# Kernel optimization log

Hardware: AMD Instinct MI355X
Metric: run time of the kernel (lower is better)

## Reference

```python
import jax, jax.numpy as jnp
import numpy as np

IMG_H, IMG_W = 512.0, 512.0
PRE_NMS = 2000   # training-mode pre_nms_top_n
POST_NMS = 2000  # training-mode post_nms_top_n
NMS_THRESH = 0.7
SCORE_THRESH = 0.0
MIN_SIZE = 0.001


def setup_inputs() -> dict:
    key = jax.random.key(0)
    k1, k2, k3 = jax.random.split(key, 3)
    N = 8
    num_anchors_per_level = (49152, 12288, 3072, 768, 192)  # strides 4..64, 3 anchors/loc on 512^2
    A = sum(num_anchors_per_level)
    cxy = jax.random.uniform(k1, (N, A, 2), minval=0.0, maxval=512.0)
    wh = jax.random.uniform(k2, (N, A, 2), minval=2.0, maxval=120.0)
    proposals = jnp.concatenate([cxy - wh / 2, cxy + wh / 2], axis=-1)  # xyxy
    objectness = jax.random.normal(k3, (N, A), dtype=jnp.float32)
    return {"proposals": proposals, "objectness": objectness,
            "num_anchors_per_level": num_anchors_per_level}


def _box_iou(a, b):
    # a: [K,4], b: [K,4] -> [K,K] pairwise IoU (torchvision box_iou semantics)
    area_a = (a[:, 2] - a[:, 0]) * (a[:, 3] - a[:, 1])
    area_b = (b[:, 2] - b[:, 0]) * (b[:, 3] - b[:, 1])
    lt = jnp.maximum(a[:, None, :2], b[None, :, :2])
    rb = jnp.minimum(a[:, None, 2:], b[None, :, 2:])
    wh = jnp.clip(rb - lt, 0.0)
    inter = wh[..., 0] * wh[..., 1]
    return inter / (area_a[:, None] + area_b[None, :] - inter)


def _per_image(boxes, scores, lvl):
    # boxes [K,4] xyxy, scores [K] (sigmoid probs), lvl [K] int32 level ids
    # 1) clip to image
    x = jnp.clip(boxes[:, 0::2], 0.0, IMG_W)
    y = jnp.clip(boxes[:, 1::2], 0.0, IMG_H)
    boxes = jnp.stack([x[:, 0], y[:, 0], x[:, 1], y[:, 1]], axis=-1)
    # 2) small-box + 3) score-threshold masks (masking instead of boolean indexing)
    ws = boxes[:, 2] - boxes[:, 0]
    hs = boxes[:, 3] - boxes[:, 1]
    valid = (ws >= MIN_SIZE) & (hs >= MIN_SIZE) & (scores >= SCORE_THRESH)
    # 4) batched NMS: offset boxes per level so levels never overlap
    off = lvl.astype(boxes.dtype) * (jnp.max(boxes) + 1.0)
    off_boxes = boxes + off[:, None]
    sm = jnp.where(valid, scores, -jnp.inf)
    order = jnp.argsort(-sm)                 # descending score, invalid last
    boxes_s = boxes[order]
    scores_s = scores[order]
    valid_s = valid[order]
    ob_s = jax.lax.stop_gradient(off_boxes[order])
    K = ob_s.shape[0]
    iou = _box_iou(ob_s, ob_s)               # [K,K], keep decision is non-differentiable
    j = jnp.arange(K)
    def body(i, keep):
        suppress = keep[i] & (iou[i] > NMS_THRESH) & (j > i)
        return keep & ~suppress
    keep = jax.lax.fori_loop(0, K, body, valid_s)
    # 5) top post_nms kept boxes, padded to fixed size with zeros
    rank = jnp.cumsum(keep.astype(jnp.int32)) - 1
    sel_key = jnp.where(keep & (rank < POST_NMS), rank, K)
    idx = jnp.argsort(sel_key)[:POST_NMS]
    out_valid = sel_key[idx] < K
    out_boxes = jnp.where(out_valid[:, None], boxes_s[idx], 0.0)
    out_scores = jnp.where(out_valid, scores_s[idx], 0.0)
    return out_boxes, out_scores


def _forward(proposals, objectness, num_anchors_per_level):
    N = proposals.shape[0]
    napl = [int(n) for n in num_anchors_per_level]
    # per-level, per-image top-k on objectness (get_top_n_idx)
    idx_list, lv_list, off = [], [], 0
    for i, n in enumerate(napl):
        k = min(PRE_NMS, n)
        _, ti = jax.lax.top_k(objectness[:, off:off + n], k)
        idx_list.append(ti + off)
        lv_list.append(jnp.full((k,), i, dtype=jnp.int32))
        off += n
    top_idx = jnp.concatenate(idx_list, axis=1)   # [N, K_total]
    lvls = jnp.concatenate(lv_list)               # [K_total], same for every image
    bidx = jnp.arange(N)[:, None]
    obj = objectness[bidx, top_idx]
    props = proposals[bidx, top_idx]
    scores = jax.nn.sigmoid(obj)
    return jax.vmap(lambda b, s: _per_image(b, s, lvls))(props, scores)


def reference(proposals, objectness, num_anchors_per_level):
    # returns (boxes [N, POST_NMS, 4], scores [N, POST_NMS]); invalid slots zero-padded
    return _forward(proposals, objectness, num_anchors_per_level)
```

## Files before the change

### kernel.cpp

```cpp
#include <hip/hip_runtime.h>
#include <math.h>

#define NIMG 8
#define ATOT 65472
#define KTOT 6960
#define POST 2000
#define TILES_PER_IMG 1668
#define NTILES (NIMG*TILES_PER_IMG)
#define ESEG 1024
#define M_TIE 0.7000000178813934326171875
#define PAD(i) ((i) + ((i) >> 5))
#define WAVE_SYNC() asm volatile("s_waitcnt lgkmcnt(0)" ::: "memory")

__constant__ int c_NAPL[5]  = {49152,12288,3072,768,192};
__constant__ int c_LOFF[5]  = {0,49152,61440,64512,65280};
__constant__ int c_KSEL[5]  = {2000,2000,2000,768,192};
__constant__ int c_CBASE[5] = {0,2000,4000,6000,6768};
__constant__ int c_GLVL[5]  = {32,32,32,12,3};
__constant__ int c_TILEPFX[6] = {0,528,1056,1584,1662,1668};

typedef float v2f __attribute__((ext_vector_type(2)));

__device__ __forceinline__ v2f vmin2(v2f a, v2f b){
#if __has_builtin(__builtin_elementwise_min)
  return __builtin_elementwise_min(a, b);
#else
  v2f r; r.x = fminf(a.x, b.x); r.y = fminf(a.y, b.y); return r;
#endif
}
__device__ __forceinline__ v2f vmax2(v2f a, v2f b){
#if __has_builtin(__builtin_elementwise_max)
  return __builtin_elementwise_max(a, b);
#else
  v2f r; r.x = fmaxf(a.x, b.x); r.y = fmaxf(a.y, b.y); return r;
#endif
}

__device__ __forceinline__ unsigned f2u(float f){
  unsigned b = __float_as_uint(f);
  return (b & 0x80000000u) ? ~b : (b | 0x80000000u);
}
__device__ __forceinline__ unsigned long long mkkey(unsigned u, unsigned gidx){
  return ((unsigned long long)u << 32) | (unsigned long long)(0xFFFFFFFFu - gidx);
}
__device__ __forceinline__ unsigned long long shflx64(unsigned long long v, int m){
  int lo = __shfl_xor((int)(unsigned)v, m);
  int hi = __shfl_xor((int)(unsigned)(v >> 32), m);
  return ((unsigned long long)(unsigned)hi << 32) | (unsigned)lo;
}
__device__ __forceinline__ unsigned long long bstep(unsigned long long v, int elem,
                                                    int size, int st){
  unsigned long long p = shflx64(v, st);
  bool lower = (elem & st) == 0;
  bool desc  = (elem & size) == 0;
  bool takeMax = (lower == desc);
  bool gt = v > p;
  return (takeMax == gt) ? v : p;
}
__device__ __forceinline__ unsigned wsuffix(unsigned v, int lane){
  #pragma unroll
  for (int off = 1; off < 64; off <<= 1){
    unsigned p = __shfl_down(v, off);
    if (lane + off < 64) v += p;
  }
  return v;
}

extern "C" __global__ void __launch_bounds__(1024)
k_select(const float* __restrict__ prop, const float* __restrict__ obj,
         unsigned long long* __restrict__ cand, float4* __restrict__ cbox,
         unsigned* __restrict__ zzone, float4* __restrict__ out4, int out_n4){
  __shared__ unsigned long long sb[2112];
  __shared__ unsigned hist[4096];
  __shared__ unsigned h8[256];
  __shared__ unsigned wsum[16];
  __shared__ unsigned s_b12, s_cumAbove, s_t20, s_cnt;
  int task = blockIdx.x, img = task/5, lvl = task%5;
  int n = c_NAPL[lvl], k = c_KSEL[lvl], tid = threadIdx.x;
  int lane = tid & 63, wv = tid >> 6;
  if (task == 0)
    for (int i = tid; i < 1280; i += 1024) zzone[i] = 0u;
  {
    int z = task*1024 + tid;
    if (z < out_n4) out4[z] = make_float4(0.f,0.f,0.f,0.f);
  }

  const float4* o4 = (const float4*)(obj + (size_t)img*ATOT + c_LOFF[lvl]);
  int n4 = n >> 2;
  unsigned kk = (unsigned)k;
  unsigned T = 0u;
  if (k < n){
    for (int i = tid; i < 4096; i += 1024) hist[i] = 0u;
    if (tid < 256) h8[tid] = 0u;
    __syncthreads();
    for (int i = tid; i < n4; i += 1024){
      float4 v = o4[i];
      atomicAdd(&hist[f2u(v.x) >> 20], 1u);
      atomicAdd(&hist[f2u(v.y) >> 20], 1u);
      atomicAdd(&hist[f2u(v.z) >> 20], 1u);
      atomicAdd(&hist[f2u(v.w) >> 20], 1u);
    }
    __syncthreads();
    unsigned own[4]; unsigned s = 0;
    int b0 = tid*4;
    #pragma unroll
    for (int j = 0; j < 4; ++j){ own[j] = hist[b0+j]; s += own[j]; }
    {
      unsigned suf = wsuffix(s, lane);
      unsigned wtot = __shfl(suf, 0);
      if (lane == 0) wsum[wv] = wtot;
      __syncthreads();
      unsigned above = 0;
      for (int w2 = wv + 1; w2 < 16; ++w2) above += wsum[w2];
      unsigned suf_incl = suf + above;
      unsigned sufn = suf_incl - s;
      #pragma unroll
      for (int j = 3; j >= 0; --j){
        unsigned sufj = sufn + own[j];
        if (sufj >= kk && sufn < kk){ s_b12 = (unsigned)(b0 + j); s_cumAbove = sufn; }
        sufn = sufj;
      }
    }
    __syncthreads();
    unsigned b12 = s_b12;
    for (int i = tid; i < n4; i += 1024){
      float4 v = o4[i];
      unsigned ux = f2u(v.x), uy = f2u(v.y), uz = f2u(v.z), uw = f2u(v.w);
      if ((ux >> 20) == b12) atomicAdd(&h8[(ux >> 12) & 255u], 1u);
      if ((uy >> 20) == b12) atomicAdd(&h8[(uy >> 12) & 255u], 1u);
      if ((uz >> 20) == b12) atomicAdd(&h8[(uz >> 12) & 255u], 1u);
      if ((uw >> 20) == b12) atomicAdd(&h8[(uw >> 12) & 255u], 1u);
    }
    __syncthreads();
    {
      unsigned hval = 0, suf8 = 0;
      if (tid < 256){
        hval = h8[tid];
        suf8 = wsuffix(hval, lane);
        if (lane == 0) wsum[wv] = suf8;
      }
      __syncthreads();
      if (tid < 256){
        unsigned above = 0;
        for (int w2 = wv + 1; w2 < 4; ++w2) above += wsum[w2];
        unsigned suf_incl = suf8 + above;
        unsigned cum = s_cumAbove;
        unsigned sufj = cum + suf_incl;
        unsigned sufn = cum + (suf_incl - hval);
        if (sufj >= kk && sufn < kk) s_t20 = (s_b12 << 8) | (unsigned)tid;
      }
    }
    __syncthreads();
    T = s_t20;
  }
  if (tid == 0) s_cnt = 0u;
  __syncthreads();
  int abase = c_LOFF[lvl];
  for (int i = tid; i < n4; i += 1024){
    float4 v = o4[i];
    float vv[4] = {v.x, v.y, v.z, v.w};
    unsigned u4[4]; bool pr4[4];
    unsigned long long bm4[4]; unsigned cw4[4];
    unsigned tot = 0;
    #pragma unroll
    for (int c2 = 0; c2 < 4; ++c2){
      u4[c2] = f2u(vv[c2]);
      pr4[c2] = (u4[c2] >> 12) >= T;
      bm4[c2] = __ballot(pr4[c2]);
      cw4[c2] = (unsigned)__popcll(bm4[c2]);
      tot += cw4[c2];
    }
    unsigned basep = 0;
    if (lane == 0 && tot) basep = atomicAdd(&s_cnt, tot);
    basep = __shfl(basep, 0);
    unsigned run = 0;
    #pragma unroll
    for (int c2 = 0; c2 < 4; ++c2){
      if (pr4[c2]){
        unsigned p = basep + run +
                     (unsigned)__popcll(bm4[c2] & ((1ull << lane) - 1ull));
        if (p < 2048u) sb[PAD(p)] = mkkey(u4[c2], (unsigned)(abase + i*4 + c2));
      }
      run += cw4[c2];
    }
  }
  __syncthreads();
  int cnt = (int)min(s_cnt, 2048u);
  int m = 256; while (m < k || m < cnt) m <<= 1;
  for (int i = cnt + tid; i < m; i += 1024) sb[PAD(i)] = 0ull;
  __syncthreads();

  int elemA = (wv << 7) | lane, elemB = elemA | 64;
  bool active = (elemA < m);
  unsigned long long va = 0ull, vb = 0ull;
  if (active){ va = sb[PAD(elemA)]; vb = sb[PAD(elemB)]; }
  if (active){
    for (int size = 2; size <= 64; size <<= 1)
      for (int st = size >> 1; st >= 1; st >>= 1){
        va = bstep(va, elemA, size, st);
        vb = bstep(vb, elemB, size, st);
      }
    {
      bool desc = ((elemA & 128) == 0);
      unsigned long long mx = (va > vb) ? va : vb;
      unsigned long long mn = (va > vb) ? vb : va;
      va = desc ? mx : mn; vb = desc ? mn : mx;
      for (int st = 32; st >= 1; st >>= 1){
        va = bstep(va, elemA, 128, st);
        vb = bstep(vb, elemB, 128, st);
      }
    }
  }
  for (int S = 256; S <= m; S <<= 1){
    if (active){ sb[PAD(elemA)] = va; sb[PAD(elemB)] = vb; }
    __syncthreads();
    for (int st = S >> 1; st >= 128; st >>= 1){
      for (int t = tid; t < (m >> 1); t += 1024){
        int lo = t & (st - 1);
        int i  = ((t - lo) << 1) + lo;
        int j  = i + st;
        bool desc = ((i & S) == 0);
        unsigned long long x = sb[PAD(i)], y = sb[PAD(j)];
        if (desc ? (x < y) : (x > y)){ sb[PAD(i)] = y; sb[PAD(j)] = x; }
      }
      __syncthreads();
    }
    if (active){
      va = sb[PAD(elemA)]; vb = sb[PAD(elemB)];
      bool desc = ((elemA & S) == 0);
      unsigned long long mx = (va > vb) ? va : vb;
      unsigned long long mn = (va > vb) ? vb : va;
      va = desc ? mx : mn; vb = desc ? mn : mx;
      for (int st = 32; st >= 1; st >>= 1){
        va = bstep(va, elemA, S, st);
        vb = bstep(vb, elemB, S, st);
      }
    }
  }
  const float4* pr = (const float4*)(prop + (size_t)img*ATOT*4);
  size_t base = (size_t)img*KTOT + c_CBASE[lvl];
  if (active){
    if (elemA < k){
      cand[base + elemA] = va;
      unsigned gidx = 0xFFFFFFFFu - (unsigned)(va & 0xFFFFFFFFull);
      float4 p = pr[gidx];
      cbox[base + elemA] = make_float4(fminf(fmaxf(p.x,0.f),512.f), fminf(fmaxf(p.y,0.f),512.f),
                                       fminf(fmaxf(p.z,0.f),512.f), fminf(fmaxf(p.w,0.f),512.f));
    }
    if (elemB < k){
      cand[base + elemB] = vb;
      unsigned gidx = 0xFFFFFFFFu - (unsigned)(vb & 0xFFFFFFFFull);
      float4 p = pr[gidx];
      cbox[base + elemB] = make_float4(fminf(fmaxf(p.x,0.f),512.f), fminf(fmaxf(p.y,0.f),512.f),
                                       fminf(fmaxf(p.z,0.f),512.f), fminf(fmaxf(p.w,0.f),512.f));
    }
  }
}

extern "C" __global__ void __launch_bounds__(256)
k_mask(const float4* __restrict__ cbox, unsigned* __restrict__ ecnt,
       unsigned* __restrict__ eseg){
  __shared__ float4 pairXY[4][32];
  __shared__ float4 pairZW[4][32];
  int tid = threadIdx.x, lane = tid & 63, wv = tid >> 6;
  int bid = blockIdx.x;
  int tile = bid*4 + wv;
  int img = tile / TILES_PER_IMG, r = tile % TILES_PER_IMG;
  int lvl = 0;
  while (r >= c_TILEPFX[lvl + 1]) ++lvl;
  int t = r - c_TILEPFX[lvl];
  int G = c_GLVL[lvl], k = c_KSEL[lvl];
  int gi = 0;
  while (t >= G - gi){ t -= G - gi; ++gi; }
  int gj = gi + t;
  int task = img*5 + lvl;
  const float4* cb = cbox + (size_t)img*KTOT + c_CBASE[lvl];

  int jj = gj*64 + lane;
  float4 bb = (jj < k) ? cb[jj] : make_float4(0.f,0.f,0.f,0.f);
  float px_ = __shfl_xor(bb.x, 1), py_ = __shfl_xor(bb.y, 1);
  float pz_ = __shfl_xor(bb.z, 1), pw_ = __shfl_xor(bb.w, 1);
  int m2 = lane >> 1;
  if ((lane & 1) == 0)
    pairXY[wv][m2] = make_float4(bb.x, px_, bb.y, py_);
  else
    pairZW[wv][m2] = make_float4(pz_, bb.z, pw_, bb.w);
  WAVE_SYNC();

  int i = gi*64 + lane;
  float4 a = cb[(i < k) ? i : (k - 1)];
  float aarea = (a.z - a.x) * (a.w - a.y);
  v2f az = {a.z, a.z}, ax = {a.x, a.x}, aw = {a.w, a.w}, ay = {a.y, a.y};
  v2f aA = {aarea, aarea};
  const float4* pxy = pairXY[wv];
  const float4* pzw = pairZW[wv];
  unsigned long long word = 0ull;
  #pragma unroll
  for (int jp = 0; jp < 32; ++jp){
    float4 q1 = pxy[jp];
    float4 q2 = pzw[jp];
    v2f bx = {q1.x, q1.y}, by = {q1.z, q1.w};
    v2f bz = {q2.x, q2.y}, bw = {q2.z, q2.w};
    v2f ix = vmin2(az, bz) - vmax2(ax, bx);
    v2f iy = vmin2(aw, bw) - vmax2(ay, by);
    v2f inter = ix * iy;
    v2f bA = (bz - bx) * (bw - by);
    v2f uni = (aA + bA) - inter;
    v2f p7 = uni * 0.7f;
    int d0 = __float_as_int(inter.x) - __float_as_int(p7.x);
    int d1 = __float_as_int(inter.y) - __float_as_int(p7.y);
    bool ov0 = (ix.x > 0.f) & (iy.x > 0.f);
    bool ov1 = (ix.y > 0.f) & (iy.y > 0.f);
    bool hit0 = ov0 & (d0 > 8);
    bool hit1 = ov1 & (d1 > 8);
    bool amb0 = ov0 & ((unsigned)(d0 + 8) <= 16u);
    bool amb1 = ov1 & ((unsigned)(d1 + 8) <= 16u);
    if (__any(amb0 | amb1)){
      if (amb0 && ((double)inter.x >= M_TIE * (double)uni.x)) hit0 = true;
      if (amb1 && ((double)inter.y >= M_TIE * (double)uni.y)) hit1 = true;
    }
    word |= (hit0 ? (1ull << (2*jp)) : 0ull) | (hit1 ? (1ull << (2*jp + 1)) : 0ull);
  }
  if (i >= k) word = 0ull;
  if (gi == gj)
    word &= (lane == 63) ? 0ull : (~0ull << (lane + 1));

  int nb = __popcll(word);
  int pfx = nb;
  for (int d = 1; d < 64; d <<= 1){
    int v = __shfl_up(pfx, d);
    if (lane >= d) pfx += v;
  }
  int total = __shfl(pfx, 63);
  if (total > 0){
    unsigned base = 0;
    if (lane == 0) base = atomicAdd(&ecnt[task*32 + gi], (unsigned)total);
    base = __shfl(base, 0);
    unsigned idx = base + (unsigned)(pfx - nb);
    unsigned* ep = eseg + (size_t)(task*32 + gi)*ESEG;
    while (word){
      int j = __ffsll(word) - 1; word &= word - 1;
      if (idx < ESEG) ep[idx] = ((unsigned)i << 16) | (unsigned)(gj*64 + j);
      ++idx;
    }
  }
}

extern "C" __global__ void __launch_bounds__(1024)
k_scan(const unsigned long long* __restrict__ cand, const unsigned* __restrict__ ecnt,
       const unsigned* __restrict__ eseg, unsigned long long* __restrict__ clist,
       unsigned* __restrict__ ccnt){
  __shared__ unsigned ledge[6144];
  __shared__ unsigned soff[33], wpfx[33];
  __shared__ unsigned long long smA[32][64];
  __shared__ unsigned long long hasIw[32];
  __shared__ unsigned long long remW[32], keepW[32];
  int task = blockIdx.x, img = task / 5, lvl = task % 5;
  int k = c_KSEL[lvl], nW = c_GLVL[lvl], tid = threadIdx.x;
  int lane = tid & 63, wv = tid >> 6;

  if (tid < 32){
    unsigned e = (tid < nW) ? min(ecnt[task*32 + tid], (unsigned)ESEG) : 0u;
    unsigned pfx = e;
    #pragma unroll
    for (int d2 = 1; d2 < 32; d2 <<= 1){
      unsigned v = __shfl_up(pfx, d2);
      if (tid >= d2) pfx += v;
    }
    soff[tid] = pfx - e;
    if (tid == 31) soff[32] = pfx;
    remW[tid] = 0ull; hasIw[tid] = 0ull;
  }
  for (int i = tid; i < 32*64; i += 1024) ((unsigned long long*)smA)[i] = 0ull;
  __syncthreads();
  for (int w = wv; w < nW; w += 16){
    unsigned c = soff[w+1] - soff[w];
    const unsigned* ep = eseg + (size_t)(task*32 + w)*ESEG;
    for (unsigned e = lane; e < c; e += 64){
      unsigned p = soff[w] + e;
      unsigned ed = ep[e];
      if (p < 6144u) ledge[p] = ed;
      int i = (int)(ed >> 16), j = (int)(ed & 0xFFFFu);
      if ((j >> 6) == w){
        atomicOr(&smA[w][i & 63], 1ull << (j & 63));
        atomicOr(&hasIw[w], 1ull << (i & 63));
      }
    }
  }
  __syncthreads();

  if (tid < 64){
    for (int w = 0; w < nW; ++w){
      unsigned long long smreg = smA[w][lane];
      unsigned long long r = remW[w];
      unsigned long long x = hasIw[w] & ~r;
      WAVE_SYNC();
      while (x){
        int i = __ffsll(x) - 1;
        unsigned rlo = __builtin_amdgcn_readlane((unsigned)smreg, i);
        unsigned rhi = __builtin_amdgcn_readlane((unsigned)(smreg >> 32), i);
        unsigned long long row = ((unsigned long long)rhi << 32) | rlo;
        r |= row;
        x &= ~(1ull << i);
        x &= ~r;
      }
      if (lane == 0) remW[w] = r;
      unsigned long long keep_w = ~r;
      unsigned c = soff[w+1] - soff[w];
      if (c){
        const unsigned* ep = eseg + (size_t)(task*32 + w)*ESEG;
        for (unsigned e = lane; e < c; e += 64){
          unsigned p = soff[w] + e;
          unsigned ed = (p < 6144u) ? ledge[p] : ep[e];
          int i = (int)(ed >> 16), j = (int)(ed & 0xFFFFu), wj = j >> 6;
          if (wj != w && ((keep_w >> (i & 63)) & 1ull))
            atomicOr(&remW[wj], 1ull << (j & 63));
        }
      }
      WAVE_SYNC();
    }
    if (lane < 32){
      unsigned long long v = 0ull;
      if (lane < nW){
        int rem = k - lane*64;
        v = (rem >= 64) ? ~0ull : ((1ull << rem) - 1ull);
      }
      keepW[lane] = v & ~remW[lane];
    }
    WAVE_SYNC();
    if (lane == 0){
      unsigned s = 0;
      for (int w = 0; w < nW; ++w){ wpfx[w] = s; s += (unsigned)__popcll(keepW[w]); }
      ccnt[task] = s;
    }
  }
  __syncthreads();
  size_t base = (size_t)img*KTOT + c_CBASE[lvl];
  for (int i = tid; i < k; i += 1024){
    unsigned long long w = keepW[i >> 6];
    if ((w >> (i & 63)) & 1ull){
      unsigned long long lowmask = (i & 63) ? ((1ull << (i & 63)) - 1ull) : 0ull;
      unsigned rank = wpfx[i >> 6] + (unsigned)__popcll(w & lowmask);
      clist[base + rank] = cand[base + i];
    }
  }
}

__device__ __forceinline__ int cntGreater(const unsigned long long* base, int len,
                                          unsigned long long x){
  int lo = 0, hi = len;
  while (lo < hi){
    int mid = (lo + hi) >> 1;
    if (base[mid] > x) lo = mid + 1; else hi = mid;
  }
  return lo;
}

extern "C" __global__ void __launch_bounds__(1024)
k_merge(const float* __restrict__ prop, const float* __restrict__ obj,
        const unsigned long long* __restrict__ clist, const unsigned* __restrict__ ccnt,
        float* __restrict__ out){
  __shared__ unsigned long long keys[KTOT];
  __shared__ int loff[6], lcnt[5];
  int img = blockIdx.x >> 3, eighth = blockIdx.x & 7, tid = threadIdx.x;
  int lane = tid & 63, wv = tid >> 6;
  if (tid < 5) lcnt[tid] = (int)ccnt[img*5 + tid];
  __syncthreads();
  if (tid == 0){
    int s = 0;
    for (int l = 0; l < 5; ++l){ loff[l] = s; s += lcnt[l]; }
    loff[5] = s;
  }
  __syncthreads();
  if (wv < 15){
    int l = wv % 5, sub = wv / 5;
    size_t gb = (size_t)img*KTOT + c_CBASE[l];
    int c = lcnt[l], lo = loff[l];
    for (int e = sub*64 + lane; e < c; e += 192) keys[lo + e] = clist[gb + e];
  }
  __syncthreads();
  const float4* pr = (const float4*)(prop + (size_t)img*ATOT*4);
  const float*  o  = obj + (size_t)img*ATOT;
  float* ob = out + (size_t)img*POST*4;
  float* os = out + (size_t)NIMG*POST*4 + (size_t)img*POST;
  int tot = loff[5];
  for (int tt = tid; ; tt += 1024){
    int t = 8*tt + eighth;
    if (t >= tot) break;
    int lvl = 0;
    while (t >= loff[lvl + 1]) ++lvl;
    unsigned long long x = keys[t];
    int pos = t - loff[lvl];
    for (int l = 0; l < 5; ++l){
      if (l == lvl) continue;
      pos += cntGreater(keys + loff[l], lcnt[l], x);
    }
    if (pos < POST){
      unsigned gidx = 0xFFFFFFFFu - (unsigned)(x & 0xFFFFFFFFull);
      float4 p = pr[gidx];
      ob[pos*4 + 0] = fminf(fmaxf(p.x, 0.f), 512.f);
      ob[pos*4 + 1] = fminf(fmaxf(p.y, 0.f), 512.f);
      ob[pos*4 + 2] = fminf(fmaxf(p.z, 0.f), 512.f);
      ob[pos*4 + 3] = fminf(fmaxf(p.w, 0.f), 512.f);
      double sgm = 1.0 / (1.0 + exp(-(double)o[gidx]));
      os[pos] = (float)sgm;
    }
  }
}

extern "C" void kernel_launch(void* const* d_in, const int* in_sizes, int n_in,
                              void* d_out, int out_size, void* d_ws, size_t ws_size,
                              hipStream_t stream){
  const float* prop = (const float*)d_in[0];
  const float* obj  = (const float*)d_in[1];
  char* ws = (char*)d_ws;
  unsigned*           ecnt = (unsigned*)(ws);
  unsigned*           ccnt = (unsigned*)(ws + 5120);
  unsigned long long* cand = (unsigned long long*)(ws + 5632);
  unsigned long long* clist= (unsigned long long*)(ws + 451072);
  float4*             cbox = (float4*)(ws + 896512);
  unsigned*           eseg = (unsigned*)(ws + 1787392);

  int out_n4 = out_size / 4;
  hipLaunchKernelGGL(k_select, dim3(40),  dim3(1024), 0, stream, prop, obj, cand, cbox,
                     ecnt, (float4*)d_out, out_n4);
  hipLaunchKernelGGL(k_mask,   dim3(NTILES/4), dim3(256), 0, stream, cbox, ecnt, eseg);
  hipLaunchKernelGGL(k_scan,   dim3(40),  dim3(1024), 0, stream, cand, ecnt, eseg, clist, ccnt);
  hipLaunchKernelGGL(k_merge,  dim3(64),  dim3(1024), 0, stream, prop, obj, clist, ccnt, (float*)d_out);
}
```

Before: 161.8 us.

## Fuse merge kernel into scan via last-block-per-image atomic counter

```diff
diff --git a/kernel.cpp b/kernel.cpp
--- a/kernel.cpp
+++ b/kernel.cpp
@@ -64,6 +64,15 @@
     if (lane + off < 64) v += p;
   }
   return v;
+}
+__device__ __forceinline__ int cntGreaterDesc(const unsigned long long* base, int len,
+                                              unsigned long long x){
+  int lo = 0, hi = len;
+  while (lo < hi){
+    int mid = (lo + hi) >> 1;
+    if (base[mid] > x) lo = mid + 1; else hi = mid;
+  }
+  return lo;
 }
 
 extern "C" __global__ void __launch_bounds__(1024)
@@ -79,7 +88,7 @@
   int n = c_NAPL[lvl], k = c_KSEL[lvl], tid = threadIdx.x;
   int lane = tid & 63, wv = tid >> 6;
   if (task == 0)
-    for (int i = tid; i < 1280; i += 1024) zzone[i] = 0u;
+    for (int i = tid; i < 1328; i += 1024) zzone[i] = 0u;
   {
     int z = task*1024 + tid;
     if (z < out_n4) out4[z] = make_float4(0.f,0.f,0.f,0.f);
@@ -347,14 +356,19 @@
 }
 
 extern "C" __global__ void __launch_bounds__(1024)
-k_scan(const unsigned long long* __restrict__ cand, const unsigned* __restrict__ ecnt,
+k_scan(const float* __restrict__ prop, const float* __restrict__ obj,
+       const unsigned long long* __restrict__ cand, const unsigned* __restrict__ ecnt,
        const unsigned* __restrict__ eseg, unsigned long long* __restrict__ clist,
-       unsigned* __restrict__ ccnt){
-  __shared__ unsigned ledge[6144];
+       unsigned* __restrict__ ccnt, unsigned* __restrict__ mdone,
+       float* __restrict__ out){
+  __shared__ unsigned long long ubuf[KTOT];
+  unsigned* ledge = (unsigned*)ubuf;
+  unsigned long long* smA = ubuf + 3072;
   __shared__ unsigned soff[33], wpfx[33];
-  __shared__ unsigned long long smA[32][64];
   __shared__ unsigned long long hasIw[32];
   __shared__ unsigned long long remW[32], keepW[32];
+  __shared__ int s_last;
+  __shared__ int loff[6], lcnt[5];
   int task = blockIdx.x, img = task / 5, lvl = task % 5;
   int k = c_KSEL[lvl], nW = c_GLVL[lvl], tid = threadIdx.x;
   int lane = tid & 63, wv = tid >> 6;
@@ -371,7 +385,7 @@
     if (tid == 31) soff[32] = pfx;
     remW[tid] = 0ull; hasIw[tid] = 0ull;
   }
-  for (int i = tid; i < 32*64; i += 1024) ((unsigned long long*)smA)[i] = 0ull;
+  for (int i = tid; i < 32*64; i += 1024) smA[i] = 0ull;
   __syncthreads();
   for (int w = wv; w < nW; w += 16){
     unsigned c = soff[w+1] - soff[w];
@@ -382,7 +396,7 @@
       if (p < 6144u) ledge[p] = ed;
       int i = (int)(ed >> 16), j = (int)(ed & 0xFFFFu);
       if ((j >> 6) == w){
-        atomicOr(&smA[w][i & 63], 1ull << (j & 63));
+        atomicOr(&smA[(w << 6) + (i & 63)], 1ull << (j & 63));
         atomicOr(&hasIw[w], 1ull << (i & 63));
       }
     }
@@ -391,7 +405,7 @@
 
   if (tid < 64){
     for (int w = 0; w < nW; ++w){
-      unsigned long long smreg = smA[w][lane];
+      unsigned long long smreg = smA[(w << 6) + lane];
       unsigned long long r = remW[w];
       unsigned long long x = hasIw[w] & ~r;
       WAVE_SYNC();
@@ -444,39 +458,31 @@
       clist[base + rank] = cand[base + i];
     }
   }
-}
-
-__device__ __forceinline__ int cntGreater(const unsigned long long* base, int len,
-                                          unsigned long long x){
-  int lo = 0, hi = len;
-  while (lo < hi){
-    int mid = (lo + hi) >> 1;
-    if (base[mid] > x) lo = mid + 1; else hi = mid;
-  }
-  return lo;
-}
-
-extern "C" __global__ void __launch_bounds__(1024)
-k_merge(const float* __restrict__ prop, const float* __restrict__ obj,
-        const unsigned long long* __restrict__ clist, const unsigned* __restrict__ ccnt,
-        float* __restrict__ out){
-  __shared__ unsigned long long keys[KTOT];
-  __shared__ int loff[6], lcnt[5];
-  int img = blockIdx.x >> 3, eighth = blockIdx.x & 7, tid = threadIdx.x;
-  int lane = tid & 63, wv = tid >> 6;
+  __syncthreads();
+
+  if (tid == 0){
+    __threadfence();
+    unsigned old = atomicAdd(&mdone[img], 1u);
+    s_last = (old == 4u) ? 1 : 0;
+  }
+  __syncthreads();
+  if (!s_last) return;
+  __threadfence();
+
+  unsigned long long* keys = ubuf;
   if (tid < 5) lcnt[tid] = (int)ccnt[img*5 + tid];
   __syncthreads();
   if (tid == 0){
-    int s = 0;
-    for (int l = 0; l < 5; ++l){ loff[l] = s; s += lcnt[l]; }
-    loff[5] = s;
+    int s2 = 0;
+    for (int l = 0; l < 5; ++l){ loff[l] = s2; s2 += lcnt[l]; }
+    loff[5] = s2;
   }
   __syncthreads();
   if (wv < 15){
     int l = wv % 5, sub = wv / 5;
     size_t gb = (size_t)img*KTOT + c_CBASE[l];
-    int c = lcnt[l], lo = loff[l];
-    for (int e = sub*64 + lane; e < c; e += 192) keys[lo + e] = clist[gb + e];
+    int c = lcnt[l], lo2 = loff[l];
+    for (int e = sub*64 + lane; e < c; e += 192) keys[lo2 + e] = clist[gb + e];
   }
   __syncthreads();
   const float4* pr = (const float4*)(prop + (size_t)img*ATOT*4);
@@ -484,16 +490,14 @@
   float* ob = out + (size_t)img*POST*4;
   float* os = out + (size_t)NIMG*POST*4 + (size_t)img*POST;
   int tot = loff[5];
-  for (int tt = tid; ; tt += 1024){
-    int t = 8*tt + eighth;
-    if (t >= tot) break;
-    int lvl = 0;
-    while (t >= loff[lvl + 1]) ++lvl;
+  for (int t = tid; t < tot; t += 1024){
+    int lv2 = 0;
+    while (t >= loff[lv2 + 1]) ++lv2;
     unsigned long long x = keys[t];
-    int pos = t - loff[lvl];
+    int pos = t - loff[lv2];
     for (int l = 0; l < 5; ++l){
-      if (l == lvl) continue;
-      pos += cntGreater(keys + loff[l], lcnt[l], x);
+      if (l == lv2) continue;
+      pos += cntGreaterDesc(keys + loff[l], lcnt[l], x);
     }
     if (pos < POST){
       unsigned gidx = 0xFFFFFFFFu - (unsigned)(x & 0xFFFFFFFFull);
@@ -516,6 +520,7 @@
   char* ws = (char*)d_ws;
   unsigned*           ecnt = (unsigned*)(ws);
   unsigned*           ccnt = (unsigned*)(ws + 5120);
+  unsigned*           mdone= (unsigned*)(ws + 5280);
   unsigned long long* cand = (unsigned long long*)(ws + 5632);
   unsigned long long* clist= (unsigned long long*)(ws + 451072);
   float4*             cbox = (float4*)(ws + 896512);
@@ -525,6 +530,6 @@
   hipLaunchKernelGGL(k_select, dim3(40),  dim3(1024), 0, stream, prop, obj, cand, cbox,
                      ecnt, (float4*)d_out, out_n4);
   hipLaunchKernelGGL(k_mask,   dim3(NTILES/4), dim3(256), 0, stream, cbox, ecnt, eseg);
-  hipLaunchKernelGGL(k_scan,   dim3(40),  dim3(1024), 0, stream, cand, ecnt, eseg, clist, ccnt);
-  hipLaunchKernelGGL(k_merge,  dim3(64),  dim3(1024), 0, stream, prop, obj, clist, ccnt, (float*)d_out);
-}
+  hipLaunchKernelGGL(k_scan,   dim3(40),  dim3(1024), 0, stream, prop, obj, cand, ecnt,
+                     eseg, clist, ccnt, mdone, (float*)d_out);
+}
```

After: 183.5 us. 13.4% more time.
